# Kernel tuning notes

Hardware: AMD Instinct MI355X
Metric: run time of the kernel (lower is better)

The kernel has to match this reference:

```python
import jax, jax.numpy as jnp
import numpy as np

N_HEADS = 8
D_HEAD = 64
IGNORE = -1.0e6  # matches the torch buffer


def setup_inputs() -> dict:
    key = jax.random.key(0)
    ks = jax.random.split(key, 9)
    B, S, D = 2, 128, 512
    H, Dh = N_HEADS, D_HEAD
    sc = lambda n: 1.0 / np.sqrt(n)
    x = jax.random.normal(ks[0], (B, S, D), jnp.float32)
    # kkq: Linear(d_model, 3*H*Dh)
    W_kkq = jax.random.normal(ks[1], (D, 3 * H * Dh), jnp.float32) * sc(D)
    b_kkq = jax.random.normal(ks[2], (3 * H * Dh,), jnp.float32) * 0.02
    # V12: Linear(2*d_model, H*Dh); split its weight into the half applied to
    # x[p] (Wv_a) and the half applied to x[s] (Wv_b) -- mathematically identical
    # to concatenating [x[p], x[s]] and applying one Linear, but avoids the
    # (B,S,S,2D) intermediate.
    Wv_a = jax.random.normal(ks[3], (D, H * Dh), jnp.float32) * sc(2 * D)
    Wv_b = jax.random.normal(ks[4], (D, H * Dh), jnp.float32) * sc(2 * D)
    b_v = jax.random.normal(ks[5], (H * Dh,), jnp.float32) * 0.02
    # Out: Linear(H*Dh, d_model)
    W_out = jax.random.normal(ks[6], (H * Dh, D), jnp.float32) * sc(H * Dh)
    b_out = jax.random.normal(ks[7], (D,), jnp.float32) * 0.02
    return {"x": x, "W_kkq": W_kkq, "b_kkq": b_kkq, "Wv_a": Wv_a,
            "Wv_b": Wv_b, "b_v": b_v, "W_out": W_out, "b_out": b_out}


def reference(x, W_kkq, b_kkq, Wv_a, Wv_b, b_v, W_out, b_out):
    B, S, D = x.shape
    H, Dh = N_HEADS, D_HEAD
    # projections
    kkq = x @ W_kkq + b_kkq                       # (B,S,3*H*Dh)
    k1, k2, q = jnp.split(kkq, 3, axis=-1)
    rs = lambda a: a.reshape(B, S, H, Dh)
    k1, k2, q = rs(k1), rs(k2), rs(q)
    # cubic tri-way scores: torch einsum 'bsnh,btnh,bqnh->bnstq' (we emit bnqst)
    scores = jnp.einsum('bsnh,btnh,bqnh->bnqst', k1, k2, q)  # (B,H,S,S,S)
    # faithful reproduction of the torch precomputed mask: only (t > q) masks
    # (the s>q term collapses to False due to the broadcast-shape bug upstream)
    idx = jnp.arange(S)
    mask_qt = idx[None, :] > idx[:, None]          # (q, t): True where t > q
    scores = jnp.where(mask_qt[None, None, :, None, :], IGNORE, scores)
    scores = scores / Dh                           # scale AFTER masking, as in torch
    # softmax jointly over the (s, t) pair axis
    A = jax.nn.softmax(scores.reshape(B, H, S, S * S), axis=-1).reshape(B, H, S, S, S)
    # values: v[p,s] = Linear([x[p], x[s]]) = x[p]@Wv_a + x[s]@Wv_b + b_v
    va = (x @ Wv_a).reshape(B, S, H, Dh)
    vb = (x @ Wv_b).reshape(B, S, H, Dh)
    # z[q] = sum_{s,t} A[q,s,t] * (va[s] + vb[t] + b_v); softmax sums to 1 so the
    # bias contributes exactly b_v
    z = (jnp.einsum('bnqst,bsnh->bqnh', A, va)
         + jnp.einsum('bnqst,btnh->bqnh', A, vb)
         + b_v.reshape(H, Dh))                     # (B,S,H,Dh)
    out = z.reshape(B, S, H * Dh) @ W_out + b_out  # (B,S,D)
    return out
```

## Files before the change

kernel.cpp:

```cpp
#include <hip/hip_runtime.h>
#include <hip/hip_bf16.h>

#define B_  2
#define S_  128
#define D_  512
#define H_  8
#define DH_ 64
#define IGNORE_VAL (-1.0e6f)
#define QB  4

#define XT_ST 72

typedef __attribute__((ext_vector_type(8))) short bf16x8;
typedef __attribute__((ext_vector_type(4))) float f32x4;

__device__ __forceinline__ unsigned short f2bf(float f) {
    unsigned int x = __float_as_uint(f);
    return (unsigned short)((x + 0x7fffu + ((x >> 16) & 1u)) >> 16);
}

__global__ __launch_bounds__(256) void proj_kernel(
    const float* __restrict__ x,
    const float* __restrict__ W_kkq, const float* __restrict__ b_kkq,
    const float* __restrict__ Wv_a,  const float* __restrict__ Wv_b,
    float* __restrict__ k1_ws, unsigned short* __restrict__ k2bf, float* __restrict__ q_ws,
    float* __restrict__ va_ws, float* __restrict__ vb_ws)
{
    __shared__ __align__(16) unsigned short xs[16 * XT_ST];
    __shared__ __align__(16) unsigned short Wt[64 * XT_ST];

    const int cb = blockIdx.x;
    const int rb = blockIdx.y;
    const int tid = threadIdx.x;
    const int lane = tid & 63, wvx = tid >> 6;
    const int n16 = lane & 15, quad = lane >> 4;

    const int part = cb >> 3;
    const float* Wbase; int wstride; int wcoloff;
    if (part <= 2) { Wbase = W_kkq; wstride = 1536; wcoloff = cb * 64; }
    else if (part == 3) { Wbase = Wv_a; wstride = 512; wcoloff = (cb - 24) * 64; }
    else { Wbase = Wv_b; wstride = 512; wcoloff = (cb - 32) * 64; }

    f32x4 acc = (f32x4){0.f, 0.f, 0.f, 0.f};

    for (int k0 = 0; k0 < D_; k0 += 64) {
        if (tid < 128) {
            const int m = tid >> 3, k8 = (tid & 7) * 8;
            const float* src = x + (size_t)(rb * 16 + m) * D_ + k0 + k8;
            const float4 a = *reinterpret_cast<const float4*>(src);
            const float4 b4 = *reinterpret_cast<const float4*>(src + 4);
            uint4 pk;
            pk.x = f2bf(a.x)  | ((unsigned)f2bf(a.y)  << 16);
            pk.y = f2bf(a.z)  | ((unsigned)f2bf(a.w)  << 16);
            pk.z = f2bf(b4.x) | ((unsigned)f2bf(b4.y) << 16);
            pk.w = f2bf(b4.z) | ((unsigned)f2bf(b4.w) << 16);
            *reinterpret_cast<uint4*>(&xs[m * XT_ST + k8]) = pk;
        }
        {
#pragma unroll
            for (int p = 0; p < 2; ++p) {
                const int kp = (tid >> 4) + p * 16;
                const int k = kp * 2;
                const int nb = (tid & 15) * 4;
                const float4 v0 = *reinterpret_cast<const float4*>(
                    Wbase + (size_t)(k0 + k) * wstride + wcoloff + nb);
                const float4 v1 = *reinterpret_cast<const float4*>(
                    Wbase + (size_t)(k0 + k + 1) * wstride + wcoloff + nb);
                *reinterpret_cast<unsigned int*>(&Wt[(nb + 0) * XT_ST + k]) =
                    f2bf(v0.x) | ((unsigned)f2bf(v1.x) << 16);
                *reinterpret_cast<unsigned int*>(&Wt[(nb + 1) * XT_ST + k]) =
                    f2bf(v0.y) | ((unsigned)f2bf(v1.y) << 16);
                *reinterpret_cast<unsigned int*>(&Wt[(nb + 2) * XT_ST + k]) =
                    f2bf(v0.z) | ((unsigned)f2bf(v1.z) << 16);
                *reinterpret_cast<unsigned int*>(&Wt[(nb + 3) * XT_ST + k]) =
                    f2bf(v0.w) | ((unsigned)f2bf(v1.w) << 16);
            }
        }
        __syncthreads();
#pragma unroll
        for (int kk = 0; kk < 2; ++kk) {
            const bf16x8 bf = *reinterpret_cast<const bf16x8*>(
                &Wt[(wvx * 16 + n16) * XT_ST + kk * 32 + quad * 8]);
            const bf16x8 af = *reinterpret_cast<const bf16x8*>(
                &xs[n16 * XT_ST + kk * 32 + quad * 8]);
            acc = __builtin_amdgcn_mfma_f32_16x16x32_bf16(af, bf, acc, 0, 0, 0);
        }
        __syncthreads();
    }

    const int n_head = cb & 7;
    const int h = wvx * 16 + n16;
    const float bias = (part <= 2) ? b_kkq[cb * 64 + h] : 0.f;
    float* Obase = (part == 0) ? k1_ws : (part == 2) ? q_ws
                 : (part == 3) ? va_ws : vb_ws;
#pragma unroll
    for (int r = 0; r < 4; ++r) {
        const int row = rb * 16 + quad * 4 + r;
        const int b = row >> 7, s = row & 127;
        const size_t o = (((size_t)(b * H_ + n_head) * S_ + s) << 6) + h;
        const float val = acc[r] + bias;
        if (part == 1) k2bf[o] = f2bf(val);
        else           Obase[o] = val;
    }
}

#define K2S 72
__global__ __launch_bounds__(256) void tri_kernel(
    const float* __restrict__ k1_ws, const unsigned short* __restrict__ k2bf,
    const float* __restrict__ q_ws,
    const float* __restrict__ va_ws, const float* __restrict__ vb_ws,
    const float* __restrict__ b_v,
    unsigned short* __restrict__ z_bf)
{
    const int qg = blockIdx.x;
    const int n = blockIdx.y;
    const int b = blockIdx.z;
    const int head = b * H_ + n;
    const float* k1h = k1_ws + (size_t)head * S_ * DH_;
    const unsigned short* k2hb = k2bf + (size_t)head * S_ * DH_;
    const float* qh = q_ws + (size_t)head * S_ * DH_;
    const float* va_h = va_ws + (size_t)head * S_ * DH_;
    const float* vb_h = vb_ws + (size_t)head * S_ * DH_;

    __shared__ __align__(16) unsigned short k2s[S_ * K2S];
    __shared__ __align__(16) float qv[QB][DH_];
    __shared__ float Asm[QB][S_];
    __shared__ float Atm[QB][S_];
    __shared__ float Atp[QB][4][S_];
    __shared__ float reds[QB][4];
    __shared__ float zred[4][QB][DH_];

    const int tid = threadIdx.x;
    const int lane = tid & 63, wv = tid >> 6;
    const int row16 = lane & 15, quad = lane >> 4;

    if (tid < QB * DH_)
        qv[tid >> 6][tid & 63] = qh[(size_t)(qg + 32 * (tid >> 6)) * DH_ + (tid & 63)];
#pragma unroll
    for (int it = 0; it < 4; ++it) {
        const int i8 = (tid + it * 256) * 8;
        const int r = i8 >> 6, c = i8 & 63;
        uint4 v = *reinterpret_cast<const uint4*>(k2hb + i8);
        *reinterpret_cast<uint4*>(&k2s[r * K2S + c]) = v;
    }

    float k1f[2][2][8];
#pragma unroll
    for (int mt = 0; mt < 2; ++mt) {
        const int srow = (wv * 2 + mt) * 16 + row16;
#pragma unroll
        for (int kk = 0; kk < 2; ++kk) {
            const int k = kk * 32 + quad * 8;
            const float4 u0 = *reinterpret_cast<const float4*>(k1h + (size_t)srow * DH_ + k);
            const float4 u1 = *reinterpret_cast<const float4*>(k1h + (size_t)srow * DH_ + k + 4);
            k1f[mt][kk][0] = u0.x; k1f[mt][kk][1] = u0.y; k1f[mt][kk][2] = u0.z; k1f[mt][kk][3] = u0.w;
            k1f[mt][kk][4] = u1.x; k1f[mt][kk][5] = u1.y; k1f[mt][kk][6] = u1.z; k1f[mt][kk][7] = u1.w;
        }
    }
    __syncthreads();

    for (int qq = 0; qq < QB; ++qq) {
        const int qidx = qg + 32 * qq;
        const int ntlim = qidx >> 4;

        bf16x8 afrag[2][2];
#pragma unroll
        for (int mt = 0; mt < 2; ++mt)
#pragma unroll
            for (int kk = 0; kk < 2; ++kk) {
                const int k = kk * 32 + quad * 8;
                bf16x8 f;
#pragma unroll
                for (int j = 0; j < 8; ++j)
                    f[j] = (short)f2bf(k1f[mt][kk][j] * qv[qq][k + j]);
                afrag[mt][kk] = f;
            }

        f32x4 acc[2][8];
#pragma unroll
        for (int mt = 0; mt < 2; ++mt)
#pragma unroll
            for (int nt = 0; nt < 8; ++nt) acc[mt][nt] = (f32x4){0.f, 0.f, 0.f, 0.f};
#pragma unroll
        for (int nt = 0; nt < 8; ++nt) {
            if (nt <= ntlim) {
#pragma unroll
                for (int kk = 0; kk < 2; ++kk) {
                    bf16x8 bfrag = *reinterpret_cast<const bf16x8*>(
                        &k2s[(nt * 16 + row16) * K2S + kk * 32 + quad * 8]);
                    acc[0][nt] = __builtin_amdgcn_mfma_f32_16x16x32_bf16(afrag[0][kk], bfrag, acc[0][nt], 0, 0, 0);
                    acc[1][nt] = __builtin_amdgcn_mfma_f32_16x16x32_bf16(afrag[1][kk], bfrag, acc[1][nt], 0, 0, 0);
                }
            }
        }

        float rs[2][4], cs[8];
#pragma unroll
        for (int nt = 0; nt < 8; ++nt) cs[nt] = 0.f;
#pragma unroll
        for (int mt = 0; mt < 2; ++mt)
#pragma unroll
            for (int r = 0; r < 4; ++r) rs[mt][r] = 0.f;
#pragma unroll
        for (int nt = 0; nt < 8; ++nt) {
            if (nt <= ntlim) {
                const int t = nt * 16 + row16;
                const bool msk = (t > qidx);
#pragma unroll
                for (int mt = 0; mt < 2; ++mt)
#pragma unroll
                    for (int r = 0; r < 4; ++r) {
                        float v = msk ? IGNORE_VAL : acc[mt][nt][r];
                        float p = __expf(v * (1.f / 64.f));
                        rs[mt][r] += p;
                        cs[nt] += p;
                    }
            }
        }

#pragma unroll
        for (int m = 1; m < 16; m <<= 1)
#pragma unroll
            for (int mt = 0; mt < 2; ++mt)
#pragma unroll
                for (int r = 0; r < 4; ++r) rs[mt][r] += __shfl_xor(rs[mt][r], m, 64);
        if (row16 == 0) {
#pragma unroll
            for (int mt = 0; mt < 2; ++mt)
#pragma unroll
                for (int r = 0; r < 4; ++r)
                    Asm[qq][(wv * 2 + mt) * 16 + quad * 4 + r] = rs[mt][r];
        }

#pragma unroll
        for (int nt = 0; nt < 8; ++nt) {
            if (nt <= ntlim) {
#pragma unroll
                for (int m = 16; m < 64; m <<= 1) cs[nt] += __shfl_xor(cs[nt], m, 64);
            }
        }
        if (quad == 0) {
#pragma unroll
            for (int nt = 0; nt < 8; ++nt) Atp[qq][wv][nt * 16 + row16] = cs[nt];
        }

        float tot = rs[0][0] + rs[0][1] + rs[0][2] + rs[0][3]
                  + rs[1][0] + rs[1][1] + rs[1][2] + rs[1][3];
#pragma unroll
        for (int m = 16; m < 64; m <<= 1) tot += __shfl_xor(tot, m, 64);
        if (lane == 0) reds[qq][wv] = tot;
    }
    __syncthreads();

    for (int i = tid; i < QB * S_; i += 256) {
        const int qq = i >> 7, t = i & 127;
        Atm[qq][t] = Atp[qq][0][t] + Atp[qq][1][t] + Atp[qq][2][t] + Atp[qq][3][t];
    }
    __syncthreads();

    {
        const int h = tid & 63, w = tid >> 6;
        float za[QB] = {0.f, 0.f, 0.f, 0.f};
        for (int i = 0; i < 32; ++i) {
            const int s = w * 32 + i;
            const float va_v = va_h[(size_t)s * DH_ + h];
            const float vb_v = vb_h[(size_t)s * DH_ + h];
#pragma unroll
            for (int qq = 0; qq < QB; ++qq)
                za[qq] += Asm[qq][s] * va_v + Atm[qq][s] * vb_v;
        }
#pragma unroll
        for (int qq = 0; qq < QB; ++qq) zred[w][qq][h] = za[qq];
    }
    __syncthreads();

    {
        const int qq = tid >> 6, h = tid & 63;
        const float Zv = reds[qq][0] + reds[qq][1] + reds[qq][2] + reds[qq][3];
        float zv = zred[0][qq][h] + zred[1][qq][h] + zred[2][qq][h] + zred[3][qq][h];
        zv = zv / Zv + b_v[n * DH_ + h];
        z_bf[((size_t)(b * S_ + qg + 32 * qq) * (H_ * DH_)) + n * DH_ + h] = f2bf(zv);
    }
}

__global__ __launch_bounds__(256) void out_kernel(
    const unsigned short* __restrict__ z_bf,
    const float* __restrict__ W_out, const float* __restrict__ b_out,
    float* __restrict__ out)
{
    __shared__ __align__(16) unsigned short zs[16 * XT_ST];
    __shared__ __align__(16) unsigned short Wt[64 * XT_ST];

    const int cb = blockIdx.x;
    const int rb = blockIdx.y;
    const int tid = threadIdx.x;
    const int lane = tid & 63, wvx = tid >> 6;
    const int n16 = lane & 15, quad = lane >> 4;

    f32x4 acc = (f32x4){0.f, 0.f, 0.f, 0.f};

    for (int k0 = 0; k0 < 512; k0 += 64) {
        {
            const int m = tid >> 4, k4 = (tid & 15) * 4;
            uint2 v = *reinterpret_cast<const uint2*>(
                z_bf + (size_t)(rb * 16 + m) * 512 + k0 + k4);
            *reinterpret_cast<uint2*>(&zs[m * XT_ST + k4]) = v;
        }
        {
#pragma unroll
            for (int p = 0; p < 2; ++p) {
                const int kp = (tid >> 4) + p * 16;
                const int k = kp * 2;
                const int nb = (tid & 15) * 4;
                const float4 v0 = *reinterpret_cast<const float4*>(
                    W_out + (size_t)(k0 + k) * 512 + cb * 64 + nb);
                const float4 v1 = *reinterpret_cast<const float4*>(
                    W_out + (size_t)(k0 + k + 1) * 512 + cb * 64 + nb);
                *reinterpret_cast<unsigned int*>(&Wt[(nb + 0) * XT_ST + k]) =
                    f2bf(v0.x) | ((unsigned)f2bf(v1.x) << 16);
                *reinterpret_cast<unsigned int*>(&Wt[(nb + 1) * XT_ST + k]) =
                    f2bf(v0.y) | ((unsigned)f2bf(v1.y) << 16);
                *reinterpret_cast<unsigned int*>(&Wt[(nb + 2) * XT_ST + k]) =
                    f2bf(v0.z) | ((unsigned)f2bf(v1.z) << 16);
                *reinterpret_cast<unsigned int*>(&Wt[(nb + 3) * XT_ST + k]) =
                    f2bf(v0.w) | ((unsigned)f2bf(v1.w) << 16);
            }
        }
        __syncthreads();
#pragma unroll
        for (int kk = 0; kk < 2; ++kk) {
            const bf16x8 bf = *reinterpret_cast<const bf16x8*>(
                &Wt[(wvx * 16 + n16) * XT_ST + kk * 32 + quad * 8]);
            const bf16x8 af = *reinterpret_cast<const bf16x8*>(
                &zs[n16 * XT_ST + kk * 32 + quad * 8]);
            acc = __builtin_amdgcn_mfma_f32_16x16x32_bf16(af, bf, acc, 0, 0, 0);
        }
        __syncthreads();
    }

    const int c = cb * 64 + wvx * 16 + n16;
    const float bias = b_out[c];
#pragma unroll
    for (int r = 0; r < 4; ++r) {
        const int row = rb * 16 + quad * 4 + r;
        out[(size_t)row * 512 + c] = acc[r] + bias;
    }
}

extern "C" void kernel_launch(void* const* d_in, const int* in_sizes, int n_in,
                              void* d_out, int out_size, void* d_ws, size_t ws_size,
                              hipStream_t stream) {
    const float* x     = (const float*)d_in[0];
    const float* W_kkq = (const float*)d_in[1];
    const float* b_kkq = (const float*)d_in[2];
    const float* Wv_a  = (const float*)d_in[3];
    const float* Wv_b  = (const float*)d_in[4];
    const float* b_v   = (const float*)d_in[5];
    const float* W_out = (const float*)d_in[6];
    const float* b_out = (const float*)d_in[7];
    float* out = (float*)d_out;

    const size_t HE = (size_t)B_ * H_ * S_ * DH_;
    float* ws = (float*)d_ws;
    float* k1_ws = ws;
    float* q_ws  = ws + HE;
    float* va_ws = ws + 2 * HE;
    float* vb_ws = ws + 3 * HE;
    unsigned short* k2bf = (unsigned short*)(ws + 4 * HE);
    unsigned short* z_bf = (unsigned short*)(ws + 4 * HE) + HE;

    proj_kernel<<<dim3(40, 16), 256, 0, stream>>>(x, W_kkq, b_kkq, Wv_a, Wv_b,
                                                  k1_ws, k2bf, q_ws, va_ws, vb_ws);
    tri_kernel<<<dim3(32, H_, B_), 256, 0, stream>>>(k1_ws, k2bf, q_ws,
                                                     va_ws, vb_ws, b_v, z_bf);
    out_kernel<<<dim3(8, 16), 256, 0, stream>>>(z_bf, W_out, b_out, out);
}
```

Before: 107.8 us.

## Fuse projection, tri-attention and output kernels into one cooperative persistent kernel

Merges the three kernel launches into a single cooperative kernel of 512 blocks that runs the projection tiles, the tri-way attention phase and the output projection, separated by grid-wide syncs. Shared memory is one union-like buffer reused across phases. The aim is to remove launch overhead and inter-kernel gaps. In exchange it adds grid.sync costs, needs occupancy of 2 blocks per CU for co-residency, and falls back to the three-kernel path if the cooperative launch fails.

```diff
diff --git a/kernel.cpp b/kernel.cpp
--- a/kernel.cpp
+++ b/kernel.cpp
@@ -1,5 +1,8 @@
 #include <hip/hip_runtime.h>
 #include <hip/hip_bf16.h>
+#include <hip/hip_cooperative_groups.h>
+
+namespace cg = cooperative_groups;
 
 #define B_  2
 #define S_  128
@@ -10,6 +13,7 @@
 #define QB  4
 
 #define XT_ST 72
+#define K2S 72
 
 typedef __attribute__((ext_vector_type(8))) short bf16x8;
 typedef __attribute__((ext_vector_type(4))) float f32x4;
@@ -19,19 +23,28 @@
     return (unsigned short)((x + 0x7fffu + ((x >> 16) & 1u)) >> 16);
 }
 
-__global__ __launch_bounds__(256) void proj_kernel(
+struct ProjLds {
+    unsigned short xs[16 * XT_ST];
+    unsigned short Wt[64 * XT_ST];
+};
+struct TriLds {
+    unsigned short k2s[S_ * K2S];
+    float qv[QB][DH_];
+    float Asm[QB][S_];
+    float Atm[QB][S_];
+    float Atp[QB][4][S_];
+    float reds[QB][4];
+    float zred[4][QB][DH_];
+};
+
+__device__ __forceinline__ void proj_tile(
+    ProjLds& L, const int cb, const int rb, const int tid,
     const float* __restrict__ x,
     const float* __restrict__ W_kkq, const float* __restrict__ b_kkq,
     const float* __restrict__ Wv_a,  const float* __restrict__ Wv_b,
     float* __restrict__ k1_ws, unsigned short* __restrict__ k2bf, float* __restrict__ q_ws,
     float* __restrict__ va_ws, float* __restrict__ vb_ws)
 {
-    __shared__ __align__(16) unsigned short xs[16 * XT_ST];
-    __shared__ __align__(16) unsigned short Wt[64 * XT_ST];
-
-    const int cb = blockIdx.x;
-    const int rb = blockIdx.y;
-    const int tid = threadIdx.x;
     const int lane = tid & 63, wvx = tid >> 6;
     const int n16 = lane & 15, quad = lane >> 4;
 
@@ -54,7 +67,7 @@
             pk.y = f2bf(a.z)  | ((unsigned)f2bf(a.w)  << 16);
             pk.z = f2bf(b4.x) | ((unsigned)f2bf(b4.y) << 16);
             pk.w = f2bf(b4.z) | ((unsigned)f2bf(b4.w) << 16);
-            *reinterpret_cast<uint4*>(&xs[m * XT_ST + k8]) = pk;
+            *reinterpret_cast<uint4*>(&L.xs[m * XT_ST + k8]) = pk;
         }
         {
 #pragma unroll
@@ -66,13 +79,13 @@
                     Wbase + (size_t)(k0 + k) * wstride + wcoloff + nb);
                 const float4 v1 = *reinterpret_cast<const float4*>(
                     Wbase + (size_t)(k0 + k + 1) * wstride + wcoloff + nb);
-                *reinterpret_cast<unsigned int*>(&Wt[(nb + 0) * XT_ST + k]) =
+                *reinterpret_cast<unsigned int*>(&L.Wt[(nb + 0) * XT_ST + k]) =
                     f2bf(v0.x) | ((unsigned)f2bf(v1.x) << 16);
-                *reinterpret_cast<unsigned int*>(&Wt[(nb + 1) * XT_ST + k]) =
+                *reinterpret_cast<unsigned int*>(&L.Wt[(nb + 1) * XT_ST + k]) =
                     f2bf(v0.y) | ((unsigned)f2bf(v1.y) << 16);
-                *reinterpret_cast<unsigned int*>(&Wt[(nb + 2) * XT_ST + k]) =
+                *reinterpret_cast<unsigned int*>(&L.Wt[(nb + 2) * XT_ST + k]) =
                     f2bf(v0.z) | ((unsigned)f2bf(v1.z) << 16);
-                *reinterpret_cast<unsigned int*>(&Wt[(nb + 3) * XT_ST + k]) =
+                *reinterpret_cast<unsigned int*>(&L.Wt[(nb + 3) * XT_ST + k]) =
                     f2bf(v0.w) | ((unsigned)f2bf(v1.w) << 16);
             }
         }
@@ -80,9 +93,9 @@
 #pragma unroll
         for (int kk = 0; kk < 2; ++kk) {
             const bf16x8 bf = *reinterpret_cast<const bf16x8*>(
-                &Wt[(wvx * 16 + n16) * XT_ST + kk * 32 + quad * 8]);
+                &L.Wt[(wvx * 16 + n16) * XT_ST + kk * 32 + quad * 8]);
             const bf16x8 af = *reinterpret_cast<const bf16x8*>(
-                &xs[n16 * XT_ST + kk * 32 + quad * 8]);
+                &L.xs[n16 * XT_ST + kk * 32 + quad * 8]);
             acc = __builtin_amdgcn_mfma_f32_16x16x32_bf16(af, bf, acc, 0, 0, 0);
         }
         __syncthreads();
@@ -104,17 +117,14 @@
     }
 }
 
-#define K2S 72
-__global__ __launch_bounds__(256) void tri_kernel(
+__device__ __forceinline__ void tri_phase(
+    TriLds& L, const int qg, const int n, const int b, const int tid,
     const float* __restrict__ k1_ws, const unsigned short* __restrict__ k2bf,
     const float* __restrict__ q_ws,
     const float* __restrict__ va_ws, const float* __restrict__ vb_ws,
     const float* __restrict__ b_v,
     unsigned short* __restrict__ z_bf)
 {
-    const int qg = blockIdx.x;
-    const int n = blockIdx.y;
-    const int b = blockIdx.z;
     const int head = b * H_ + n;
     const float* k1h = k1_ws + (size_t)head * S_ * DH_;
     const unsigned short* k2hb = k2bf + (size_t)head * S_ * DH_;
@@ -122,26 +132,17 @@
     const float* va_h = va_ws + (size_t)head * S_ * DH_;
     const float* vb_h = vb_ws + (size_t)head * S_ * DH_;
 
-    __shared__ __align__(16) unsigned short k2s[S_ * K2S];
-    __shared__ __align__(16) float qv[QB][DH_];
-    __shared__ float Asm[QB][S_];
-    __shared__ float Atm[QB][S_];
-    __shared__ float Atp[QB][4][S_];
-    __shared__ float reds[QB][4];
-    __shared__ float zred[4][QB][DH_];
-
-    const int tid = threadIdx.x;
     const int lane = tid & 63, wv = tid >> 6;
     const int row16 = lane & 15, quad = lane >> 4;
 
     if (tid < QB * DH_)
-        qv[tid >> 6][tid & 63] = qh[(size_t)(qg + 32 * (tid >> 6)) * DH_ + (tid & 63)];
+        L.qv[tid >> 6][tid & 63] = qh[(size_t)(qg + 32 * (tid >> 6)) * DH_ + (tid & 63)];
 #pragma unroll
     for (int it = 0; it < 4; ++it) {
         const int i8 = (tid + it * 256) * 8;
         const int r = i8 >> 6, c = i8 & 63;
         uint4 v = *reinterpret_cast<const uint4*>(k2hb + i8);
-        *reinterpret_cast<uint4*>(&k2s[r * K2S + c]) = v;
+        *reinterpret_cast<uint4*>(&L.k2s[r * K2S + c]) = v;
     }
 
     float k1f[2][2][8];
@@ -172,7 +173,7 @@
                 bf16x8 f;
 #pragma unroll
                 for (int j = 0; j < 8; ++j)
-                    f[j] = (short)f2bf(k1f[mt][kk][j] * qv[qq][k + j]);
+                    f[j] = (short)f2bf(k1f[mt][kk][j] * L.qv[qq][k + j]);
                 afrag[mt][kk] = f;
             }
 
@@ -187,7 +188,7 @@
 #pragma unroll
                 for (int kk = 0; kk < 2; ++kk) {
                     bf16x8 bfrag = *reinterpret_cast<const bf16x8*>(
-                        &k2s[(nt * 16 + row16) * K2S + kk * 32 + quad * 8]);
+                        &L.k2s[(nt * 16 + row16) * K2S + kk * 32 + quad * 8]);
                     acc[0][nt] = __builtin_amdgcn_mfma_f32_16x16x32_bf16(afrag[0][kk], bfrag, acc[0][nt], 0, 0, 0);
                     acc[1][nt] = __builtin_amdgcn_mfma_f32_16x16x32_bf16(afrag[1][kk], bfrag, acc[1][nt], 0, 0, 0);
                 }
@@ -229,7 +230,7 @@
             for (int mt = 0; mt < 2; ++mt)
 #pragma unroll
                 for (int r = 0; r < 4; ++r)
-                    Asm[qq][(wv * 2 + mt) * 16 + quad * 4 + r] = rs[mt][r];
+                    L.Asm[qq][(wv * 2 + mt) * 16 + quad * 4 + r] = rs[mt][r];
         }
 
 #pragma unroll
@@ -241,20 +242,20 @@
         }
         if (quad == 0) {
 #pragma unroll
-            for (int nt = 0; nt < 8; ++nt) Atp[qq][wv][nt * 16 + row16] = cs[nt];
+            for (int nt = 0; nt < 8; ++nt) L.Atp[qq][wv][nt * 16 + row16] = cs[nt];
         }
 
         float tot = rs[0][0] + rs[0][1] + rs[0][2] + rs[0][3]
                   + rs[1][0] + rs[1][1] + rs[1][2] + rs[1][3];
 #pragma unroll
         for (int m = 16; m < 64; m <<= 1) tot += __shfl_xor(tot, m, 64);
-        if (lane == 0) reds[qq][wv] = tot;
+        if (lane == 0) L.reds[qq][wv] = tot;
     }
     __syncthreads();
 
     for (int i = tid; i < QB * S_; i += 256) {
         const int qq = i >> 7, t = i & 127;
-        Atm[qq][t] = Atp[qq][0][t] + Atp[qq][1][t] + Atp[qq][2][t] + Atp[qq][3][t];
+        L.Atm[qq][t] = L.Atp[qq][0][t] + L.Atp[qq][1][t] + L.Atp[qq][2][t] + L.Atp[qq][3][t];
     }
     __syncthreads();
 
@@ -267,33 +268,28 @@
             const float vb_v = vb_h[(size_t)s * DH_ + h];
 #pragma unroll
             for (int qq = 0; qq < QB; ++qq)
-                za[qq] += Asm[qq][s] * va_v + Atm[qq][s] * vb_v;
-        }
-#pragma unroll
-        for (int qq = 0; qq < QB; ++qq) zred[w][qq][h] = za[qq];
+                za[qq] += L.Asm[qq][s] * va_v + L.Atm[qq][s] * vb_v;
+        }
+#pragma unroll
+        for (int qq = 0; qq < QB; ++qq) L.zred[w][qq][h] = za[qq];
     }
     __syncthreads();
 
     {
         const int qq = tid >> 6, h = tid & 63;
-        const float Zv = reds[qq][0] + reds[qq][1] + reds[qq][2] + reds[qq][3];
-        float zv = zred[0][qq][h] + zred[1][qq][h] + zred[2][qq][h] + zred[3][qq][h];
+        const float Zv = L.reds[qq][0] + L.reds[qq][1] + L.reds[qq][2] + L.reds[qq][3];
+        float zv = L.zred[0][qq][h] + L.zred[1][qq][h] + L.zred[2][qq][h] + L.zred[3][qq][h];
         zv = zv / Zv + b_v[n * DH_ + h];
         z_bf[((size_t)(b * S_ + qg + 32 * qq) * (H_ * DH_)) + n * DH_ + h] = f2bf(zv);
     }
 }
 
-__global__ __launch_bounds__(256) void out_kernel(
+__device__ __forceinline__ void out_tile(
+    ProjLds& L, const int cb, const int rb, const int tid,
     const unsigned short* __restrict__ z_bf,
     const float* __restrict__ W_out, const float* __restrict__ b_out,
     float* __restrict__ out)
 {
-    __shared__ __align__(16) unsigned short zs[16 * XT_ST];
-    __shared__ __align__(16) unsigned short Wt[64 * XT_ST];
-
-    const int cb = blockIdx.x;
-    const int rb = blockIdx.y;
-    const int tid = threadIdx.x;
     const int lane = tid & 63, wvx = tid >> 6;
     const int n16 = lane & 15, quad = lane >> 4;
 
@@ -304,7 +300,7 @@
             const int m = tid >> 4, k4 = (tid & 15) * 4;
             uint2 v = *reinterpret_cast<const uint2*>(
                 z_bf + (size_t)(rb * 16 + m) * 512 + k0 + k4);
-            *reinterpret_cast<uint2*>(&zs[m * XT_ST + k4]) = v;
+            *reinterpret_cast<uint2*>(&L.xs[m * XT_ST + k4]) = v;
         }
         {
 #pragma unroll
@@ -316,13 +312,13 @@
                     W_out + (size_t)(k0 + k) * 512 + cb * 64 + nb);
                 const float4 v1 = *reinterpret_cast<const float4*>(
                     W_out + (size_t)(k0 + k + 1) * 512 + cb * 64 + nb);
-                *reinterpret_cast<unsigned int*>(&Wt[(nb + 0) * XT_ST + k]) =
+                *reinterpret_cast<unsigned int*>(&L.Wt[(nb + 0) * XT_ST + k]) =
                     f2bf(v0.x) | ((unsigned)f2bf(v1.x) << 16);
-                *reinterpret_cast<unsigned int*>(&Wt[(nb + 1) * XT_ST + k]) =
+                *reinterpret_cast<unsigned int*>(&L.Wt[(nb + 1) * XT_ST + k]) =
                     f2bf(v0.y) | ((unsigned)f2bf(v1.y) << 16);
-                *reinterpret_cast<unsigned int*>(&Wt[(nb + 2) * XT_ST + k]) =
+                *reinterpret_cast<unsigned int*>(&L.Wt[(nb + 2) * XT_ST + k]) =
                     f2bf(v0.z) | ((unsigned)f2bf(v1.z) << 16);
-                *reinterpret_cast<unsigned int*>(&Wt[(nb + 3) * XT_ST + k]) =
+                *reinterpret_cast<unsigned int*>(&L.Wt[(nb + 3) * XT_ST + k]) =
                     f2bf(v0.w) | ((unsigned)f2bf(v1.w) << 16);
             }
         }
@@ -330,9 +326,9 @@
 #pragma unroll
         for (int kk = 0; kk < 2; ++kk) {
             const bf16x8 bf = *reinterpret_cast<const bf16x8*>(
-                &Wt[(wvx * 16 + n16) * XT_ST + kk * 32 + quad * 8]);
+                &L.Wt[(wvx * 16 + n16) * XT_ST + kk * 32 + quad * 8]);
             const bf16x8 af = *reinterpret_cast<const bf16x8*>(
-                &zs[n16 * XT_ST + kk * 32 + quad * 8]);
+                &L.xs[n16 * XT_ST + kk * 32 + quad * 8]);
             acc = __builtin_amdgcn_mfma_f32_16x16x32_bf16(af, bf, acc, 0, 0, 0);
         }
         __syncthreads();
@@ -345,6 +341,80 @@
         const int row = rb * 16 + quad * 4 + r;
         out[(size_t)row * 512 + c] = acc[r] + bias;
     }
+}
+
+__global__ __launch_bounds__(256, 2) void fused_kernel(
+    const float* __restrict__ x,
+    const float* __restrict__ W_kkq, const float* __restrict__ b_kkq,
+    const float* __restrict__ Wv_a,  const float* __restrict__ Wv_b,
+    const float* __restrict__ b_v,
+    const float* __restrict__ W_out, const float* __restrict__ b_out,
+    float* __restrict__ out,
+    float* __restrict__ k1_ws, unsigned short* __restrict__ k2bf, float* __restrict__ q_ws,
+    float* __restrict__ va_ws, float* __restrict__ vb_ws,
+    unsigned short* __restrict__ z_bf)
+{
+    __shared__ __align__(16) unsigned char smem_raw[sizeof(TriLds)];
+    const int tid = threadIdx.x;
+    const int bid = blockIdx.x;
+    cg::grid_group grid = cg::this_grid();
+
+    {
+        ProjLds& L = *reinterpret_cast<ProjLds*>(smem_raw);
+        for (int tile = bid; tile < 640; tile += 512) {
+            const int cb = tile % 40, rb = tile / 40;
+            proj_tile(L, cb, rb, tid, x, W_kkq, b_kkq, Wv_a, Wv_b,
+                      k1_ws, k2bf, q_ws, va_ws, vb_ws);
+            __syncthreads();
+        }
+    }
+    grid.sync();
+
+    {
+        TriLds& L = *reinterpret_cast<TriLds*>(smem_raw);
+        tri_phase(L, bid & 31, (bid >> 5) & 7, bid >> 8, tid,
+                  k1_ws, k2bf, q_ws, va_ws, vb_ws, b_v, z_bf);
+    }
+    grid.sync();
+
+    if (bid < 128) {
+        ProjLds& L = *reinterpret_cast<ProjLds*>(smem_raw);
+        out_tile(L, bid & 7, bid >> 3, tid, z_bf, W_out, b_out, out);
+    }
+}
+
+__global__ __launch_bounds__(256) void proj_kernel(
+    const float* __restrict__ x,
+    const float* __restrict__ W_kkq, const float* __restrict__ b_kkq,
+    const float* __restrict__ Wv_a,  const float* __restrict__ Wv_b,
+    float* __restrict__ k1_ws, unsigned short* __restrict__ k2bf, float* __restrict__ q_ws,
+    float* __restrict__ va_ws, float* __restrict__ vb_ws)
+{
+    __shared__ __align__(16) unsigned char sm[sizeof(ProjLds)];
+    proj_tile(*reinterpret_cast<ProjLds*>(sm), blockIdx.x, blockIdx.y, threadIdx.x,
+              x, W_kkq, b_kkq, Wv_a, Wv_b, k1_ws, k2bf, q_ws, va_ws, vb_ws);
+}
+
+__global__ __launch_bounds__(256) void tri_kernel(
+    const float* __restrict__ k1_ws, const unsigned short* __restrict__ k2bf,
+    const float* __restrict__ q_ws,
+    const float* __restrict__ va_ws, const float* __restrict__ vb_ws,
+    const float* __restrict__ b_v,
+    unsigned short* __restrict__ z_bf)
+{
+    __shared__ __align__(16) unsigned char sm[sizeof(TriLds)];
+    tri_phase(*reinterpret_cast<TriLds*>(sm), blockIdx.x, blockIdx.y, blockIdx.z,
+              threadIdx.x, k1_ws, k2bf, q_ws, va_ws, vb_ws, b_v, z_bf);
+}
+
+__global__ __launch_bounds__(256) void out_kernel(
+    const unsigned short* __restrict__ z_bf,
+    const float* __restrict__ W_out, const float* __restrict__ b_out,
+    float* __restrict__ out)
+{
+    __shared__ __align__(16) unsigned char sm[sizeof(ProjLds)];
+    out_tile(*reinterpret_cast<ProjLds*>(sm), blockIdx.x, blockIdx.y, threadIdx.x,
+             z_bf, W_out, b_out, out);
 }
 
 extern "C" void kernel_launch(void* const* d_in, const int* in_sizes, int n_in,
@@ -369,9 +439,32 @@
     unsigned short* k2bf = (unsigned short*)(ws + 4 * HE);
     unsigned short* z_bf = (unsigned short*)(ws + 4 * HE) + HE;
 
-    proj_kernel<<<dim3(40, 16), 256, 0, stream>>>(x, W_kkq, b_kkq, Wv_a, Wv_b,
-                                                  k1_ws, k2bf, q_ws, va_ws, vb_ws);
-    tri_kernel<<<dim3(32, H_, B_), 256, 0, stream>>>(k1_ws, k2bf, q_ws,
-                                                     va_ws, vb_ws, b_v, z_bf);
-    out_kernel<<<dim3(8, 16), 256, 0, stream>>>(z_bf, W_out, b_out, out);
-}
+    void* kargs[15];
+    kargs[0]  = (void*)&x;
+    kargs[1]  = (void*)&W_kkq;
+    kargs[2]  = (void*)&b_kkq;
+    kargs[3]  = (void*)&Wv_a;
+    kargs[4]  = (void*)&Wv_b;
+    kargs[5]  = (void*)&b_v;
+    kargs[6]  = (void*)&W_out;
+    kargs[7]  = (void*)&b_out;
+    kargs[8]  = (void*)&out;
+    kargs[9]  = (void*)&k1_ws;
+    kargs[10] = (void*)&k2bf;
+    kargs[11] = (void*)&q_ws;
+    kargs[12] = (void*)&va_ws;
+    kargs[13] = (void*)&vb_ws;
+    kargs[14] = (void*)&z_bf;
+
+    hipError_t err = hipLaunchCooperativeKernel(
+        reinterpret_cast<const void*>(&fused_kernel),
+        dim3(512), dim3(256), kargs, 0, stream);
+
+    if (err != hipSuccess) {
+        proj_kernel<<<dim3(40, 16), 256, 0, stream>>>(x, W_kkq, b_kkq, Wv_a, Wv_b,
+                                                      k1_ws, k2bf, q_ws, va_ws, vb_ws);
+        tri_kernel<<<dim3(32, H_, B_), 256, 0, stream>>>(k1_ws, k2bf, q_ws,
+                                                         va_ws, vb_ws, b_v, z_bf);
+        out_kernel<<<dim3(8, 16), 256, 0, stream>>>(z_bf, W_out, b_out, out);
+    }
+}
```

Result: slower. 221.4 us (+105.4%).

## Stage full activation rows once and load weights directly into MFMA registers

Applied to the files above, without the earlier changes.

In proj_kernel and out_kernel, the whole 16x512 activation tile is now staged in shared memory once, before a single barrier. Weight B-fragments are read straight from global memory into registers, with strided scalar loads converted to bf16 on the fly. This removes the per-k-step shared-memory staging of weights and the two barriers per iteration. The cost is uncoalesced-looking scalar global loads: each lane reads 8 strided floats, although lanes within a row are contiguous across n16. It also uses a larger shared-memory footprint for the activation tile.

```diff
diff --git a/kernel.cpp b/kernel.cpp
--- a/kernel.cpp
+++ b/kernel.cpp
@@ -9,7 +9,8 @@
 #define IGNORE_VAL (-1.0e6f)
 #define QB  4
 
-#define XT_ST 72
+#define XSF 520
+#define K2S 72
 
 typedef __attribute__((ext_vector_type(8))) short bf16x8;
 typedef __attribute__((ext_vector_type(4))) float f32x4;
@@ -26,8 +27,7 @@
     float* __restrict__ k1_ws, unsigned short* __restrict__ k2bf, float* __restrict__ q_ws,
     float* __restrict__ va_ws, float* __restrict__ vb_ws)
 {
-    __shared__ __align__(16) unsigned short xs[16 * XT_ST];
-    __shared__ __align__(16) unsigned short Wt[64 * XT_ST];
+    __shared__ __align__(16) unsigned short xs[16 * XSF];
 
     const int cb = blockIdx.x;
     const int rb = blockIdx.y;
@@ -41,12 +41,12 @@
     else if (part == 3) { Wbase = Wv_a; wstride = 512; wcoloff = (cb - 24) * 64; }
     else { Wbase = Wv_b; wstride = 512; wcoloff = (cb - 32) * 64; }
 
-    f32x4 acc = (f32x4){0.f, 0.f, 0.f, 0.f};
-
-    for (int k0 = 0; k0 < D_; k0 += 64) {
-        if (tid < 128) {
-            const int m = tid >> 3, k8 = (tid & 7) * 8;
-            const float* src = x + (size_t)(rb * 16 + m) * D_ + k0 + k8;
+    {
+        const int c = (tid & 63) * 8;
+#pragma unroll
+        for (int i = 0; i < 4; ++i) {
+            const int m = (tid >> 6) + i * 4;
+            const float* src = x + (size_t)(rb * 16 + m) * D_ + c;
             const float4 a = *reinterpret_cast<const float4*>(src);
             const float4 b4 = *reinterpret_cast<const float4*>(src + 4);
             uint4 pk;
@@ -54,38 +54,27 @@
             pk.y = f2bf(a.z)  | ((unsigned)f2bf(a.w)  << 16);
             pk.z = f2bf(b4.x) | ((unsigned)f2bf(b4.y) << 16);
             pk.w = f2bf(b4.z) | ((unsigned)f2bf(b4.w) << 16);
-            *reinterpret_cast<uint4*>(&xs[m * XT_ST + k8]) = pk;
-        }
-        {
-#pragma unroll
-            for (int p = 0; p < 2; ++p) {
-                const int kp = (tid >> 4) + p * 16;
-                const int k = kp * 2;
-                const int nb = (tid & 15) * 4;
-                const float4 v0 = *reinterpret_cast<const float4*>(
-                    Wbase + (size_t)(k0 + k) * wstride + wcoloff + nb);
-                const float4 v1 = *reinterpret_cast<const float4*>(
-                    Wbase + (size_t)(k0 + k + 1) * wstride + wcoloff + nb);
-                *reinterpret_cast<unsigned int*>(&Wt[(nb + 0) * XT_ST + k]) =
-                    f2bf(v0.x) | ((unsigned)f2bf(v1.x) << 16);
-                *reinterpret_cast<unsigned int*>(&Wt[(nb + 1) * XT_ST + k]) =
-                    f2bf(v0.y) | ((unsigned)f2bf(v1.y) << 16);
-                *reinterpret_cast<unsigned int*>(&Wt[(nb + 2) * XT_ST + k]) =
-                    f2bf(v0.z) | ((unsigned)f2bf(v1.z) << 16);
-                *reinterpret_cast<unsigned int*>(&Wt[(nb + 3) * XT_ST + k]) =
-                    f2bf(v0.w) | ((unsigned)f2bf(v1.w) << 16);
-            }
-        }
-        __syncthreads();
+            *reinterpret_cast<uint4*>(&xs[m * XSF + c]) = pk;
+        }
+    }
+    __syncthreads();
+
+    f32x4 acc = (f32x4){0.f, 0.f, 0.f, 0.f};
+    const int ncol = wcoloff + wvx * 16 + n16;
+
+#pragma unroll
+    for (int ks = 0; ks < 8; ++ks) {
 #pragma unroll
         for (int kk = 0; kk < 2; ++kk) {
-            const bf16x8 bf = *reinterpret_cast<const bf16x8*>(
-                &Wt[(wvx * 16 + n16) * XT_ST + kk * 32 + quad * 8]);
-            const bf16x8 af = *reinterpret_cast<const bf16x8*>(
-                &xs[n16 * XT_ST + kk * 32 + quad * 8]);
+            const int k = ks * 64 + kk * 32 + quad * 8;
+            const float* wp = Wbase + (size_t)k * wstride + ncol;
+            bf16x8 bf;
+#pragma unroll
+            for (int j = 0; j < 8; ++j)
+                bf[j] = (short)f2bf(wp[(size_t)j * wstride]);
+            const bf16x8 af = *reinterpret_cast<const bf16x8*>(&xs[n16 * XSF + k]);
             acc = __builtin_amdgcn_mfma_f32_16x16x32_bf16(af, bf, acc, 0, 0, 0);
         }
-        __syncthreads();
     }
 
     const int n_head = cb & 7;
@@ -104,7 +93,6 @@
     }
 }
 
-#define K2S 72
 __global__ __launch_bounds__(256) void tri_kernel(
     const float* __restrict__ k1_ws, const unsigned short* __restrict__ k2bf,
     const float* __restrict__ q_ws,
@@ -288,8 +276,7 @@
     const float* __restrict__ W_out, const float* __restrict__ b_out,
     float* __restrict__ out)
 {
-    __shared__ __align__(16) unsigned short zs[16 * XT_ST];
-    __shared__ __align__(16) unsigned short Wt[64 * XT_ST];
+    __shared__ __align__(16) unsigned short zs[16 * XSF];
 
     const int cb = blockIdx.x;
     const int rb = blockIdx.y;
@@ -297,53 +284,41 @@
     const int lane = tid & 63, wvx = tid >> 6;
     const int n16 = lane & 15, quad = lane >> 4;
 
+    {
+        const int c = (tid & 63) * 8;
+#pragma unroll
+        for (int i = 0; i < 4; ++i) {
+            const int m = (tid >> 6) + i * 4;
+            uint4 v = *reinterpret_cast<const uint4*>(
+                z_bf + (size_t)(rb * 16 + m) * 512 + c);
+            *reinterpret_cast<uint4*>(&zs[m * XSF + c]) = v;
+        }
+    }
+    __syncthreads();
+
     f32x4 acc = (f32x4){0.f, 0.f, 0.f, 0.f};
-
-    for (int k0 = 0; k0 < 512; k0 += 64) {
-        {
-            const int m = tid >> 4, k4 = (tid & 15) * 4;
-            uint2 v = *reinterpret_cast<const uint2*>(
-                z_bf + (size_t)(rb * 16 + m) * 512 + k0 + k4);
-            *reinterpret_cast<uint2*>(&zs[m * XT_ST + k4]) = v;
-        }
-        {
-#pragma unroll
-            for (int p = 0; p < 2; ++p) {
-                const int kp = (tid >> 4) + p * 16;
-                const int k = kp * 2;
-                const int nb = (tid & 15) * 4;
-                const float4 v0 = *reinterpret_cast<const float4*>(
-                    W_out + (size_t)(k0 + k) * 512 + cb * 64 + nb);
-                const float4 v1 = *reinterpret_cast<const float4*>(
-                    W_out + (size_t)(k0 + k + 1) * 512 + cb * 64 + nb);
-                *reinterpret_cast<unsigned int*>(&Wt[(nb + 0) * XT_ST + k]) =
-                    f2bf(v0.x) | ((unsigned)f2bf(v1.x) << 16);
-                *reinterpret_cast<unsigned int*>(&Wt[(nb + 1) * XT_ST + k]) =
-                    f2bf(v0.y) | ((unsigned)f2bf(v1.y) << 16);
-                *reinterpret_cast<unsigned int*>(&Wt[(nb + 2) * XT_ST + k]) =
-                    f2bf(v0.z) | ((unsigned)f2bf(v1.z) << 16);
-                *reinterpret_cast<unsigned int*>(&Wt[(nb + 3) * XT_ST + k]) =
-                    f2bf(v0.w) | ((unsigned)f2bf(v1.w) << 16);
-            }
-        }
-        __syncthreads();
+    const int ncol = cb * 64 + wvx * 16 + n16;
+
+#pragma unroll
+    for (int ks = 0; ks < 8; ++ks) {
 #pragma unroll
         for (int kk = 0; kk < 2; ++kk) {
-            const bf16x8 bf = *reinterpret_cast<const bf16x8*>(
-                &Wt[(wvx * 16 + n16) * XT_ST + kk * 32 + quad * 8]);
-            const bf16x8 af = *reinterpret_cast<const bf16x8*>(
-                &zs[n16 * XT_ST + kk * 32 + quad * 8]);
+            const int k = ks * 64 + kk * 32 + quad * 8;
+            const float* wp = W_out + (size_t)k * 512 + ncol;
+            bf16x8 bf;
+#pragma unroll
+            for (int j = 0; j < 8; ++j)
+                bf[j] = (short)f2bf(wp[(size_t)j * 512]);
+            const bf16x8 af = *reinterpret_cast<const bf16x8*>(&zs[n16 * XSF + k]);
             acc = __builtin_amdgcn_mfma_f32_16x16x32_bf16(af, bf, acc, 0, 0, 0);
         }
-        __syncthreads();
-    }
-
-    const int c = cb * 64 + wvx * 16 + n16;
-    const float bias = b_out[c];
+    }
+
+    const float bias = b_out[ncol];
 #pragma unroll
     for (int r = 0; r < 4; ++r) {
         const int row = rb * 16 + quad * 4 + r;
-        out[(size_t)row * 512 + c] = acc[r] + bias;
+        out[(size_t)row * 512 + ncol] = acc[r] + bias;
     }
 }
 
```

Result: faster. 102.1 us (-5.3%).
